# Kernel optimization log

Hardware: AMD Instinct MI355X
Metric: run time of the kernel (lower is better)

## Reference

```python
import jax, jax.numpy as jnp
import numpy as np

H = 32          # num query heads
KV = 8          # num kv heads
D = 64          # head_dim
WIN = 512       # sliding_window
BASE = 10000.0  # rope base


def setup_inputs() -> dict:
    key = jax.random.key(0)
    ks = jax.random.split(key, 5)
    B, S, DIM = 2, 2048, 2048
    x = jax.random.normal(ks[0], (B, S, DIM), dtype=jnp.float32)
    wq = jax.random.normal(ks[1], (H * D, DIM), dtype=jnp.float32) * 0.02
    wk = jax.random.normal(ks[2], (KV * D, DIM), dtype=jnp.float32) * 0.02
    wv = jax.random.normal(ks[3], (KV * D, DIM), dtype=jnp.float32) * 0.02
    wo = jax.random.normal(ks[4], (DIM, H * D), dtype=jnp.float32) * 0.02
    return {"x": x, "wq": wq, "wk": wk, "wv": wv, "wo": wo}


def _rope_tables(S):
    inv_freq = 1.0 / (BASE ** (jnp.arange(0, D, 2, dtype=jnp.float32) / D))
    t = jnp.arange(S, dtype=jnp.float32)
    freqs = t[:, None] * inv_freq[None, :]          # [S, D/2]
    emb = jnp.concatenate([freqs, freqs], axis=-1)  # [S, D]
    return jnp.cos(emb)[:, None, :], jnp.sin(emb)[:, None, :]  # [S,1,D]


def _rotate_half(u):
    return jnp.concatenate([-u[..., D // 2:], u[..., :D // 2]], axis=-1)


def reference(x, wq, wk, wv, wo):
    B, S, _ = x.shape
    q = (x @ wq.T).reshape(B, S, H, D)
    k = (x @ wk.T).reshape(B, S, KV, D)
    v = (x @ wv.T).reshape(B, S, KV, D)

    cos, sin = _rope_tables(S)  # [S,1,D] broadcasts over batch and heads
    q = q * cos + _rotate_half(q) * sin
    k = k * cos + _rotate_half(k) * sin

    q = q.transpose(0, 2, 1, 3)                        # [B,H,S,D]
    k = jnp.repeat(k.transpose(0, 2, 1, 3), H // KV, axis=1)  # [B,H,S,D]
    v = jnp.repeat(v.transpose(0, 2, 1, 3), H // KV, axis=1)

    scale = 1.0 / jnp.sqrt(jnp.float32(D))
    scores = jnp.einsum('bhqd,bhkd->bhqk', q, k) * scale  # [B,H,S,S]

    i = jnp.arange(S)[:, None]
    j = jnp.arange(S)[None, :]
    window_mask = jnp.abs(i - j) > WIN // 2   # True = masked (outside window)
    causal_mask = j > i                        # True = masked (future)
    masked = window_mask | causal_mask
    scores = jnp.where(masked[None, None], -jnp.inf, scores)

    attn = jax.nn.softmax(scores, axis=-1)
    out = jnp.einsum('bhqk,bhkd->bhqd', attn, v)  # [B,H,S,D]
    out = out.transpose(0, 2, 1, 3).reshape(B, S, H * D)
    return out @ wo.T
```

## Files before the change

kernel.cpp:

```cpp
#include <hip/hip_runtime.h>
#include <cstdint>
#include <cstddef>

#define SLEN 2048
#define NB 2
#define NH 32
#define NKV 8
#define HD 64
#define MROWS 4096
#define QDIM 2048
#define KVDIM 512
#define WINH 256

typedef float f32x4 __attribute__((ext_vector_type(4)));
typedef __bf16 bf16x8 __attribute__((ext_vector_type(8)));

__device__ __forceinline__ unsigned short f2bf(float f) {
  union { float f; unsigned u; } v; v.f = f;
  unsigned r = v.u + 0x7fffu + ((v.u >> 16) & 1u);
  return (unsigned short)(r >> 16);
}
__device__ __forceinline__ float bf2f(unsigned short h) {
  union { unsigned u; float f; } v; v.u = ((unsigned)h) << 16;
  return v.f;
}
__device__ __forceinline__ unsigned pk2(float a, float b) {
  return (unsigned)f2bf(a) | ((unsigned)f2bf(b) << 16);
}
__device__ __forceinline__ uint4 cvt16(float4 a, float4 b) {
  uint4 u;
  u.x = pk2(a.x, a.y); u.y = pk2(a.z, a.w);
  u.z = pk2(b.x, b.y); u.w = pk2(b.z, b.w);
  return u;
}
__device__ __forceinline__ void async16(const unsigned short* g, unsigned short* l) {
  __builtin_amdgcn_global_load_lds(
      (const __attribute__((address_space(1))) unsigned int*)g,
      (__attribute__((address_space(3))) unsigned int*)l, 16, 0, 0);
}

__global__ void rope_table(float2* __restrict__ tab) {
  int tid = blockIdx.x * 256 + threadIdx.x;
  int d = tid & 31;
  int s = tid >> 5;
  float inv = expf((float)d * (-2.0f / 64.0f) * 9.210340371976184f);
  float ang = (float)s * inv;
  float sn, cs;
  sincosf(ang, &sn, &cs);
  tab[tid] = make_float2(cs, sn);
}

__global__ void conv_bf16(const float* __restrict__ src, unsigned short* __restrict__ dst) {
  size_t t = (size_t)blockIdx.x * 256 + threadIdx.x;
  float4 a = *(const float4*)(src + t * 8);
  float4 b = *(const float4*)(src + t * 8 + 4);
  *(uint4*)(dst + t * 8) = cvt16(a, b);
}

__global__ void conv_wqkv(const float* __restrict__ wq, const float* __restrict__ wk,
                          const float* __restrict__ wv, unsigned short* __restrict__ dst) {
  size_t t = (size_t)blockIdx.x * 256 + threadIdx.x;
  size_t e = t * 8;
  int row = (int)(e >> 11);
  const float* src; size_t off;
  if (row < 2048)       { src = wq; off = e; }
  else if (row < 2560)  { src = wk; off = e - (size_t)2048 * 2048; }
  else                  { src = wv; off = e - (size_t)2560 * 2048; }
  float4 a = *(const float4*)(src + off);
  float4 b = *(const float4*)(src + off + 4);
  *(uint4*)(dst + e) = cvt16(a, b);
}

__global__ __launch_bounds__(512, 2) void qkv_gemm(
    const unsigned short* __restrict__ Ap, const unsigned short* __restrict__ Bp,
    const float* __restrict__ tabf,
    unsigned short* __restrict__ o_q, unsigned short* __restrict__ o_k,
    unsigned short* __restrict__ o_v)
{
  extern __shared__ unsigned short L[];
  constexpr int NT = 32;

  const int bid = blockIdx.x;
  const int swz = (bid & 7) * 24 + (bid >> 3);
  const int bm0 = (swz & 15) * 256;
  const int bn0 = (swz >> 4) * 256;

  const int tid = threadIdx.x;
  const int lane = tid & 63, wid = tid >> 6;
  const int g = lane >> 4, cl = lane & 15;
  const int wm = wid >> 2, wn = wid & 3;

  const int r0 = wid * 32 + (lane >> 2);
  const int s0 = (((lane & 3) ^ ((lane >> 3) & 3)) << 3);
  const unsigned short* gA = Ap + (size_t)(bm0 + r0) * 2048 + s0;
  const unsigned short* gB = Bp + (size_t)(bn0 + r0) * 2048 + s0;

  const int slotus = ((g ^ ((cl >> 1) & 3)) << 3);
  const int aread = (wm * 128 + cl) * 32 + slotus;
  const int bread = (wn * 64 + cl) * 32 + slotus;

#define REG_(b, op, kh) ((((b) * 2 + (op)) * 2 + (kh)) * 8192)
#define STG(op, kh, tt, db) do { \
    const unsigned short* s_ = ((op) ? gB : gA) + (tt) * 64 + (kh) * 32; \
    unsigned short* d_ = L + REG_(db, op, kh) + wid * 1024; \
    async16(s_, d_); \
    async16(s_ + 16 * 2048, d_ + 512); \
  } while (0)
#define LDA(dst, kh, mh) \
    _Pragma("unroll") for (int mf = 0; mf < 4; ++mf) \
      dst[mf] = *(const bf16x8*)&L[REG_(cb, 0, kh) + aread + (mh) * 2048 + mf * 512];
#define LDB(dst, kh) \
    _Pragma("unroll") for (int nf = 0; nf < 4; ++nf) \
      dst[nf] = *(const bf16x8*)&L[REG_(cb, 1, kh) + bread + nf * 512];
#define MM(mh, A, B) do { \
    __builtin_amdgcn_s_setprio(1); \
    _Pragma("unroll") for (int mf = 0; mf < 4; ++mf) \
      _Pragma("unroll") for (int nf = 0; nf < 4; ++nf) \
        acc[(mh) * 4 + mf][nf] = __builtin_amdgcn_mfma_f32_16x16x32_bf16( \
            A[mf], B[nf], acc[(mh) * 4 + mf][nf], 0, 0, 0); \
    __builtin_amdgcn_s_setprio(0); \
  } while (0)

  f32x4 acc[8][4] = {};

  STG(0, 0, 0, 0); STG(1, 0, 0, 0); STG(0, 1, 0, 0); STG(1, 1, 0, 0);
  STG(0, 0, 1, 1); STG(1, 0, 1, 1);
  asm volatile("s_waitcnt vmcnt(4)" ::: "memory");
  __builtin_amdgcn_s_barrier();
  __builtin_amdgcn_sched_barrier(0);

#pragma unroll 1
  for (int t = 0; t < NT; ++t) {
    const int cb = t & 1, nb = cb ^ 1;
    bf16x8 a00[4], a10[4], a01[4], a11[4], b0[4], b1[4];

    if (t + 1 < NT) STG(0, 1, t + 1, nb);
    LDA(a00, 0, 0); LDB(b0, 0);
    if (t + 1 < NT) STG(1, 1, t + 1, nb);
    LDA(a10, 0, 1);
    MM(0, a00, b0);
    LDA(a01, 1, 0); LDB(b1, 1);
    MM(1, a10, b0);
    asm volatile("s_waitcnt lgkmcnt(0)" ::: "memory");
    __builtin_amdgcn_s_barrier();
    __builtin_amdgcn_sched_barrier(0);
    if (t + 2 < NT) STG(0, 0, t + 2, cb);
    LDA(a11, 1, 1);
    MM(0, a01, b1);
    if (t + 2 < NT) STG(1, 0, t + 2, cb);
    MM(1, a11, b1);
    if (t + 2 < NT) { asm volatile("s_waitcnt vmcnt(4)" ::: "memory"); }
    else            { asm volatile("s_waitcnt vmcnt(0)" ::: "memory"); }
    asm volatile("s_waitcnt lgkmcnt(0)" ::: "memory");
    __builtin_amdgcn_s_barrier();
    __builtin_amdgcn_sched_barrier(0);
  }
#undef MM
#undef LDB
#undef LDA
#undef STG
#undef REG_

  const int rb = bm0 + wm * 128;
  const float2* tab = (const float2*)tabf;
  if (bn0 < QDIM) {
    const int colb = bn0 + wn * 64;
#pragma unroll
    for (int m = 0; m < 8; ++m)
#pragma unroll
      for (int nf = 0; nf < 2; ++nf) {
        const int d = nf * 16 + cl;
#pragma unroll
        for (int p = 0; p < 4; ++p) {
          int row = rb + m * 16 + g * 4 + p;
          int s = row & (SLEN - 1);
          float2 cs = tab[s * 32 + d];
          float a = acc[m][nf][p], b2 = acc[m][nf + 2][p];
          o_q[(size_t)row * QDIM + colb + d]      = f2bf(a * cs.x - b2 * cs.y);
          o_q[(size_t)row * QDIM + colb + d + 32] = f2bf(b2 * cs.x + a * cs.y);
        }
      }
  } else if (bn0 < QDIM + KVDIM) {
    const int colb = bn0 - QDIM + wn * 64;
#pragma unroll
    for (int m = 0; m < 8; ++m)
#pragma unroll
      for (int nf = 0; nf < 2; ++nf) {
        const int d = nf * 16 + cl;
#pragma unroll
        for (int p = 0; p < 4; ++p) {
          int row = rb + m * 16 + g * 4 + p;
          int s = row & (SLEN - 1);
          float2 cs = tab[s * 32 + d];
          float a = acc[m][nf][p], b2 = acc[m][nf + 2][p];
          o_k[(size_t)row * KVDIM + colb + d]      = f2bf(a * cs.x - b2 * cs.y);
          o_k[(size_t)row * KVDIM + colb + d + 32] = f2bf(b2 * cs.x + a * cs.y);
        }
      }
  } else {
    const int colb = bn0 - QDIM - KVDIM + wn * 64;
#pragma unroll
    for (int m = 0; m < 8; ++m)
#pragma unroll
      for (int nf = 0; nf < 4; ++nf) {
        int col = colb + nf * 16 + cl;
        int kvh = col >> 6, d = col & 63;
        int row0 = rb + m * 16 + g * 4;
        int bb = row0 >> 11, s = row0 & (SLEN - 1);
        unsigned short* dst = o_v + (((size_t)(bb * NKV + kvh) * HD + d) << 11) + s;
        uint2 u;
        u.x = pk2(acc[m][nf][0], acc[m][nf][1]);
        u.y = pk2(acc[m][nf][2], acc[m][nf][3]);
        *(uint2*)dst = u;
      }
  }
}

__global__ __launch_bounds__(512, 2) void out_gemm(
    const unsigned short* __restrict__ Ap, const unsigned short* __restrict__ Bp,
    float* __restrict__ o_f)
{
  extern __shared__ unsigned short L[];
  constexpr int NT = 32;

  const int bid = blockIdx.x;
  const int swz = (bid & 7) * 32 + (bid >> 3);
  const int bm0 = (swz & 31) * 128;
  const int bn0 = (swz >> 5) * 256;

  const int tid = threadIdx.x;
  const int lane = tid & 63, wid = tid >> 6;
  const int g = lane >> 4, cl = lane & 15;
  const int wm = wid >> 2, wn = wid & 3;

  const int s0 = (((lane & 3) ^ ((lane >> 3) & 3)) << 3);
  const unsigned short* gA = Ap + (size_t)(bm0 + wid * 16 + (lane >> 2)) * 2048 + s0;
  const unsigned short* gB = Bp + (size_t)(bn0 + wid * 32 + (lane >> 2)) * 2048 + s0;

  const int slotus = ((g ^ ((cl >> 1) & 3)) << 3);
  const int aread = (wm * 64 + cl) * 32 + slotus;
  const int bread = (wn * 64 + cl) * 32 + slotus;

#define REGA_(b, kh) ((b) * 24576 + (kh) * 4096)
#define REGB_(b, kh) ((b) * 24576 + 8192 + (kh) * 8192)
#define STGA(kh, tt, db) \
    async16(gA + (tt) * 64 + (kh) * 32, L + REGA_(db, kh) + wid * 512)
#define STGB(kh, tt, db) do { \
    const unsigned short* s_ = gB + (tt) * 64 + (kh) * 32; \
    unsigned short* d_ = L + REGB_(db, kh) + wid * 1024; \
    async16(s_, d_); \
    async16(s_ + 16 * 2048, d_ + 512); \
  } while (0)
#define LA(dst, kh, mp) \
    _Pragma("unroll") for (int mf = 0; mf < 2; ++mf) \
      dst[mf] = *(const bf16x8*)&L[REGA_(cb, kh) + aread + (mp) * 1024 + mf * 512];
#define LB(dst, kh) \
    _Pragma("unroll") for (int nf = 0; nf < 4; ++nf) \
      dst[nf] = *(const bf16x8*)&L[REGB_(cb, kh) + bread + nf * 512];
#define MMO(mp, A, B) do { \
    __builtin_amdgcn_s_setprio(1); \
    _Pragma("unroll") for (int mf = 0; mf < 2; ++mf) \
      _Pragma("unroll") for (int nf = 0; nf < 4; ++nf) \
        acc[(mp) * 2 + mf][nf] = __builtin_amdgcn_mfma_f32_16x16x32_bf16( \
            A[mf], B[nf], acc[(mp) * 2 + mf][nf], 0, 0, 0); \
    __builtin_amdgcn_s_setprio(0); \
  } while (0)

  f32x4 acc[4][4] = {};

  STGA(0, 0, 0); STGB(0, 0, 0); STGA(1, 0, 0); STGB(1, 0, 0);
  STGA(0, 1, 1); STGB(0, 1, 1);
  asm volatile("s_waitcnt vmcnt(3)" ::: "memory");
  __builtin_amdgcn_s_barrier();
  __builtin_amdgcn_sched_barrier(0);

#pragma unroll 1
  for (int t = 0; t < NT; ++t) {
    const int cb = t & 1, nb = cb ^ 1;
    bf16x8 p00[2], p10[2], p01[2], p11[2], b0[4], b1[4];

    if (t + 1 < NT) STGA(1, t + 1, nb);
    LA(p00, 0, 0); LB(b0, 0);
    if (t + 1 < NT) STGB(1, t + 1, nb);
    LA(p10, 0, 1);
    MMO(0, p00, b0);
    LA(p01, 1, 0); LB(b1, 1);
    MMO(1, p10, b0);
    asm volatile("s_waitcnt lgkmcnt(0)" ::: "memory");
    __builtin_amdgcn_s_barrier();
    __builtin_amdgcn_sched_barrier(0);
    if (t + 2 < NT) STGA(0, t + 2, cb);
    LA(p11, 1, 1);
    MMO(0, p01, b1);
    if (t + 2 < NT) STGB(0, t + 2, cb);
    MMO(1, p11, b1);
    if (t + 2 < NT) { asm volatile("s_waitcnt vmcnt(3)" ::: "memory"); }
    else            { asm volatile("s_waitcnt vmcnt(0)" ::: "memory"); }
    asm volatile("s_waitcnt lgkmcnt(0)" ::: "memory");
    __builtin_amdgcn_s_barrier();
    __builtin_amdgcn_sched_barrier(0);
  }
#undef MMO
#undef LB
#undef LA
#undef STGB
#undef STGA
#undef REGB_
#undef REGA_

  const int rb = bm0 + wm * 64;
  const int colb = bn0 + wn * 64;
#pragma unroll
  for (int m = 0; m < 4; ++m)
#pragma unroll
    for (int nf = 0; nf < 4; ++nf)
#pragma unroll
      for (int p = 0; p < 4; ++p) {
        int row = rb + m * 16 + g * 4 + p;
        o_f[(size_t)row * 2048 + colb + nf * 16 + cl] = acc[m][nf][p];
      }
}

__global__ __launch_bounds__(256) void attn(
    const unsigned short* __restrict__ qb, const unsigned short* __restrict__ kb,
    const unsigned short* __restrict__ vt, unsigned short* __restrict__ ao)
{
  __shared__ __align__(16) unsigned short Plds[4][16][40];
  const int lane = threadIdx.x & 63, wid = threadIdx.x >> 6;
  const int g = lane >> 4, cl = lane & 15;
  const int qt = blockIdx.x * 4 + wid;
  const int bh = qt >> 7, tl = qt & 127;
  const int i0 = tl * 16;
  const int b = bh >> 5, h = bh & 31, kvh = (bh & 31) >> 2;
  const int qi = i0 + cl;

  const unsigned short* qp = qb + ((size_t)(b * SLEN + i0 + cl) * NH + h) * HD + g * 8;
  bf16x8 qf0 = *(const bf16x8*)qp;
  bf16x8 qf1 = *(const bf16x8*)(qp + 32);

  f32x4 acc_o[4] = {};
  float m_run = -1e30f, l_run = 0.f;
  int jb = i0 - WINH; if (jb < 0) jb = 0;

  for (int j0 = jb; j0 <= i0; j0 += 32) {
    f32x4 sacc[2];
#pragma unroll
    for (int t = 0; t < 2; ++t) {
      int krow = j0 + 16 * t + cl;
      if (krow > SLEN - 1) krow = SLEN - 1;
      const unsigned short* kp = kb + ((size_t)(b * SLEN + krow) * NKV + kvh) * HD + g * 8;
      bf16x8 kf0 = *(const bf16x8*)kp;
      bf16x8 kf1 = *(const bf16x8*)(kp + 32);
      f32x4 z = {};
      z = __builtin_amdgcn_mfma_f32_16x16x32_bf16(kf0, qf0, z, 0, 0, 0);
      z = __builtin_amdgcn_mfma_f32_16x16x32_bf16(kf1, qf1, z, 0, 0, 0);
      sacc[t] = z;
    }
    float s[2][4];
    float mx = -1e30f;
#pragma unroll
    for (int t = 0; t < 2; ++t)
#pragma unroll
      for (int p = 0; p < 4; ++p) {
        int kj = j0 + 16 * t + g * 4 + p;
        bool ok = (kj <= qi) && (qi - kj <= WINH);
        float v = ok ? sacc[t][p] * 0.125f : -1e30f;
        s[t][p] = v;
        mx = fmaxf(mx, v);
      }
    mx = fmaxf(mx, __shfl_xor(mx, 16));
    mx = fmaxf(mx, __shfl_xor(mx, 32));
    float mnew = fmaxf(m_run, mx);
    float corr = __expf(m_run - mnew);
    float ps = 0.f;
    unsigned pw[2][2];
#pragma unroll
    for (int t = 0; t < 2; ++t) {
      float p0 = __expf(s[t][0] - mnew);
      float p1 = __expf(s[t][1] - mnew);
      float p2 = __expf(s[t][2] - mnew);
      float p3 = __expf(s[t][3] - mnew);
      ps += p0 + p1 + p2 + p3;
      pw[t][0] = pk2(p0, p1);
      pw[t][1] = pk2(p2, p3);
    }
    ps += __shfl_xor(ps, 16);
    ps += __shfl_xor(ps, 32);
    l_run = l_run * corr + ps;
    m_run = mnew;
#pragma unroll
    for (int vbk = 0; vbk < 4; ++vbk)
#pragma unroll
      for (int p = 0; p < 4; ++p) acc_o[vbk][p] *= corr;
#pragma unroll
    for (int t = 0; t < 2; ++t) {
      *(unsigned*)&Plds[wid][cl][16 * t + 4 * g]     = pw[t][0];
      *(unsigned*)&Plds[wid][cl][16 * t + 4 * g + 2] = pw[t][1];
    }
    bf16x8 pf = *(const bf16x8*)&Plds[wid][cl][g * 8];
    int jv = j0 + g * 8;
    if (jv > SLEN - 8) jv = SLEN - 8;
    const unsigned short* vbase = vt + ((size_t)(b * NKV + kvh) * HD) * SLEN + jv;
#pragma unroll
    for (int vbk = 0; vbk < 4; ++vbk) {
      bf16x8 vf = *(const bf16x8*)(vbase + (size_t)(vbk * 16 + cl) * SLEN);
      acc_o[vbk] = __builtin_amdgcn_mfma_f32_16x16x32_bf16(vf, pf, acc_o[vbk], 0, 0, 0);
    }
  }
  float inv = 1.0f / l_run;
  unsigned short* op = ao + ((size_t)(b * SLEN + i0 + cl) * NH + h) * HD;
#pragma unroll
  for (int vbk = 0; vbk < 4; ++vbk) {
    unsigned u0 = pk2(acc_o[vbk][0] * inv, acc_o[vbk][1] * inv);
    unsigned u1 = pk2(acc_o[vbk][2] * inv, acc_o[vbk][3] * inv);
    *(unsigned*)(op + vbk * 16 + g * 4)     = u0;
    *(unsigned*)(op + vbk * 16 + g * 4 + 2) = u1;
  }
}

extern "C" void kernel_launch(void* const* d_in, const int* in_sizes, int n_in,
                              void* d_out, int out_size, void* d_ws, size_t ws_size,
                              hipStream_t stream) {
  const float* x  = (const float*)d_in[0];
  const float* wq = (const float*)d_in[1];
  const float* wk = (const float*)d_in[2];
  const float* wv = (const float*)d_in[3];
  const float* wo = (const float*)d_in[4];
  float* out = (float*)d_out;

  char* w = (char*)d_ws;
  unsigned short* wqkvb = (unsigned short*)w; w += (size_t)3072 * 2048 * 2;
  unsigned short* xb    = (unsigned short*)w; w += (size_t)MROWS * QDIM * 2;
  unsigned short* qb    = (unsigned short*)w; w += (size_t)MROWS * QDIM * 2;
  unsigned short* kb    = (unsigned short*)w; w += (size_t)MROWS * KVDIM * 2;
  unsigned short* vt    = (unsigned short*)w; w += (size_t)MROWS * KVDIM * 2;
  float* tab            = (float*)w;          w += (size_t)SLEN * 32 * 8;
  unsigned short* wob = wqkvb;
  unsigned short* ao  = xb;

  hipFuncSetAttribute((const void*)qkv_gemm,
                      hipFuncAttributeMaxDynamicSharedMemorySize, 131072);
  hipFuncSetAttribute((const void*)out_gemm,
                      hipFuncAttributeMaxDynamicSharedMemorySize, 98304);

  rope_table<<<SLEN * 32 / 256, 256, 0, stream>>>((float2*)tab);
  conv_bf16<<<(MROWS * 2048) / (8 * 256), 256, 0, stream>>>(x, xb);
  conv_wqkv<<<(3072 * 2048) / (8 * 256), 256, 0, stream>>>(wq, wk, wv, wqkvb);
  qkv_gemm<<<192, 512, 131072, stream>>>(xb, wqkvb, tab, qb, kb, vt);
  conv_bf16<<<(2048 * 2048) / (8 * 256), 256, 0, stream>>>(wo, wob);
  attn<<<(NB * NH * (SLEN / 16)) / 4, 256, 0, stream>>>(qb, kb, vt, ao);
  out_gemm<<<256, 512, 98304, stream>>>(ao, wob, out);
}
```

Baseline: 194.7 us.

## Shrink QKV and output GEMM tiles to 128x128 with 256-thread blocks

Both GEMMs move from 256x256 (QKV) and 128x256 (output) tiles with 512-thread blocks to uniform 128x128 tiles with 256-thread blocks and 64 KB LDS. This raises the grid from 192 and 256 blocks to 768 and 512, so the work fills all CUs of the MI355X more evenly. The inner loop is simplified to two A/B fragment loads per k-step, and one lgkmcnt wait is removed. The cost is less data reuse per tile, so each output element needs more global and LDS traffic.

```diff
diff --git a/kernel.cpp b/kernel.cpp
--- a/kernel.cpp
+++ b/kernel.cpp
@@ -71,7 +71,7 @@
   *(uint4*)(dst + e) = cvt16(a, b);
 }
 
-__global__ __launch_bounds__(512, 2) void qkv_gemm(
+__global__ __launch_bounds__(256, 2) void qkv_gemm(
     const unsigned short* __restrict__ Ap, const unsigned short* __restrict__ Bp,
     const float* __restrict__ tabf,
     unsigned short* __restrict__ o_q, unsigned short* __restrict__ o_k,
@@ -81,14 +81,14 @@
   constexpr int NT = 32;
 
   const int bid = blockIdx.x;
-  const int swz = (bid & 7) * 24 + (bid >> 3);
-  const int bm0 = (swz & 15) * 256;
-  const int bn0 = (swz >> 4) * 256;
+  const int swz = (bid & 7) * 96 + (bid >> 3);
+  const int bm0 = (swz & 31) * 128;
+  const int bn0 = (swz >> 5) * 128;
 
   const int tid = threadIdx.x;
   const int lane = tid & 63, wid = tid >> 6;
   const int g = lane >> 4, cl = lane & 15;
-  const int wm = wid >> 2, wn = wid & 3;
+  const int wm = wid >> 1, wn = wid & 1;
 
   const int r0 = wid * 32 + (lane >> 2);
   const int s0 = (((lane & 3) ^ ((lane >> 3) & 3)) << 3);
@@ -96,32 +96,32 @@
   const unsigned short* gB = Bp + (size_t)(bn0 + r0) * 2048 + s0;
 
   const int slotus = ((g ^ ((cl >> 1) & 3)) << 3);
-  const int aread = (wm * 128 + cl) * 32 + slotus;
+  const int aread = (wm * 64 + cl) * 32 + slotus;
   const int bread = (wn * 64 + cl) * 32 + slotus;
 
-#define REG_(b, op, kh) ((((b) * 2 + (op)) * 2 + (kh)) * 8192)
+#define REG_(b, op, kh) ((((b) * 2 + (op)) * 2 + (kh)) * 4096)
 #define STG(op, kh, tt, db) do { \
     const unsigned short* s_ = ((op) ? gB : gA) + (tt) * 64 + (kh) * 32; \
     unsigned short* d_ = L + REG_(db, op, kh) + wid * 1024; \
     async16(s_, d_); \
     async16(s_ + 16 * 2048, d_ + 512); \
   } while (0)
-#define LDA(dst, kh, mh) \
+#define LDA(dst, kh) \
     _Pragma("unroll") for (int mf = 0; mf < 4; ++mf) \
-      dst[mf] = *(const bf16x8*)&L[REG_(cb, 0, kh) + aread + (mh) * 2048 + mf * 512];
+      dst[mf] = *(const bf16x8*)&L[REG_(cb, 0, kh) + aread + mf * 512];
 #define LDB(dst, kh) \
     _Pragma("unroll") for (int nf = 0; nf < 4; ++nf) \
       dst[nf] = *(const bf16x8*)&L[REG_(cb, 1, kh) + bread + nf * 512];
-#define MM(mh, A, B) do { \
+#define MM(A, B) do { \
     __builtin_amdgcn_s_setprio(1); \
     _Pragma("unroll") for (int mf = 0; mf < 4; ++mf) \
       _Pragma("unroll") for (int nf = 0; nf < 4; ++nf) \
-        acc[(mh) * 4 + mf][nf] = __builtin_amdgcn_mfma_f32_16x16x32_bf16( \
-            A[mf], B[nf], acc[(mh) * 4 + mf][nf], 0, 0, 0); \
+        acc[mf][nf] = __builtin_amdgcn_mfma_f32_16x16x32_bf16( \
+            A[mf], B[nf], acc[mf][nf], 0, 0, 0); \
     __builtin_amdgcn_s_setprio(0); \
   } while (0)
 
-  f32x4 acc[8][4] = {};
+  f32x4 acc[4][4] = {};
 
   STG(0, 0, 0, 0); STG(1, 0, 0, 0); STG(0, 1, 0, 0); STG(1, 1, 0, 0);
   STG(0, 0, 1, 1); STG(1, 0, 1, 1);
@@ -132,26 +132,21 @@
 #pragma unroll 1
   for (int t = 0; t < NT; ++t) {
     const int cb = t & 1, nb = cb ^ 1;
-    bf16x8 a00[4], a10[4], a01[4], a11[4], b0[4], b1[4];
+    bf16x8 a0[4], a1[4], b0[4], b1[4];
 
     if (t + 1 < NT) STG(0, 1, t + 1, nb);
-    LDA(a00, 0, 0); LDB(b0, 0);
+    LDA(a0, 0); LDB(b0, 0);
     if (t + 1 < NT) STG(1, 1, t + 1, nb);
-    LDA(a10, 0, 1);
-    MM(0, a00, b0);
-    LDA(a01, 1, 0); LDB(b1, 1);
-    MM(1, a10, b0);
+    LDA(a1, 1); LDB(b1, 1);
+    MM(a0, b0);
     asm volatile("s_waitcnt lgkmcnt(0)" ::: "memory");
     __builtin_amdgcn_s_barrier();
     __builtin_amdgcn_sched_barrier(0);
     if (t + 2 < NT) STG(0, 0, t + 2, cb);
-    LDA(a11, 1, 1);
-    MM(0, a01, b1);
+    MM(a1, b1);
     if (t + 2 < NT) STG(1, 0, t + 2, cb);
-    MM(1, a11, b1);
     if (t + 2 < NT) { asm volatile("s_waitcnt vmcnt(4)" ::: "memory"); }
     else            { asm volatile("s_waitcnt vmcnt(0)" ::: "memory"); }
-    asm volatile("s_waitcnt lgkmcnt(0)" ::: "memory");
     __builtin_amdgcn_s_barrier();
     __builtin_amdgcn_sched_barrier(0);
   }
@@ -161,12 +156,12 @@
 #undef STG
 #undef REG_
 
-  const int rb = bm0 + wm * 128;
+  const int rb = bm0 + wm * 64;
   const float2* tab = (const float2*)tabf;
   if (bn0 < QDIM) {
     const int colb = bn0 + wn * 64;
 #pragma unroll
-    for (int m = 0; m < 8; ++m)
+    for (int m = 0; m < 4; ++m)
 #pragma unroll
       for (int nf = 0; nf < 2; ++nf) {
         const int d = nf * 16 + cl;
@@ -183,7 +178,7 @@
   } else if (bn0 < QDIM + KVDIM) {
     const int colb = bn0 - QDIM + wn * 64;
 #pragma unroll
-    for (int m = 0; m < 8; ++m)
+    for (int m = 0; m < 4; ++m)
 #pragma unroll
       for (int nf = 0; nf < 2; ++nf) {
         const int d = nf * 16 + cl;
@@ -200,7 +195,7 @@
   } else {
     const int colb = bn0 - QDIM - KVDIM + wn * 64;
 #pragma unroll
-    for (int m = 0; m < 8; ++m)
+    for (int m = 0; m < 4; ++m)
 #pragma unroll
       for (int nf = 0; nf < 4; ++nf) {
         int col = colb + nf * 16 + cl;
@@ -216,7 +211,7 @@
   }
 }
 
-__global__ __launch_bounds__(512, 2) void out_gemm(
+__global__ __launch_bounds__(256, 2) void out_gemm(
     const unsigned short* __restrict__ Ap, const unsigned short* __restrict__ Bp,
     float* __restrict__ o_f)
 {
@@ -224,89 +219,80 @@
   constexpr int NT = 32;
 
   const int bid = blockIdx.x;
-  const int swz = (bid & 7) * 32 + (bid >> 3);
+  const int swz = (bid & 7) * 64 + (bid >> 3);
   const int bm0 = (swz & 31) * 128;
-  const int bn0 = (swz >> 5) * 256;
+  const int bn0 = (swz >> 5) * 128;
 
   const int tid = threadIdx.x;
   const int lane = tid & 63, wid = tid >> 6;
   const int g = lane >> 4, cl = lane & 15;
-  const int wm = wid >> 2, wn = wid & 3;
-
+  const int wm = wid >> 1, wn = wid & 1;
+
+  const int r0 = wid * 32 + (lane >> 2);
   const int s0 = (((lane & 3) ^ ((lane >> 3) & 3)) << 3);
-  const unsigned short* gA = Ap + (size_t)(bm0 + wid * 16 + (lane >> 2)) * 2048 + s0;
-  const unsigned short* gB = Bp + (size_t)(bn0 + wid * 32 + (lane >> 2)) * 2048 + s0;
+  const unsigned short* gA = Ap + (size_t)(bm0 + r0) * 2048 + s0;
+  const unsigned short* gB = Bp + (size_t)(bn0 + r0) * 2048 + s0;
 
   const int slotus = ((g ^ ((cl >> 1) & 3)) << 3);
   const int aread = (wm * 64 + cl) * 32 + slotus;
   const int bread = (wn * 64 + cl) * 32 + slotus;
 
-#define REGA_(b, kh) ((b) * 24576 + (kh) * 4096)
-#define REGB_(b, kh) ((b) * 24576 + 8192 + (kh) * 8192)
-#define STGA(kh, tt, db) \
-    async16(gA + (tt) * 64 + (kh) * 32, L + REGA_(db, kh) + wid * 512)
-#define STGB(kh, tt, db) do { \
-    const unsigned short* s_ = gB + (tt) * 64 + (kh) * 32; \
-    unsigned short* d_ = L + REGB_(db, kh) + wid * 1024; \
+#define REG_(b, op, kh) ((((b) * 2 + (op)) * 2 + (kh)) * 4096)
+#define STG(op, kh, tt, db) do { \
+    const unsigned short* s_ = ((op) ? gB : gA) + (tt) * 64 + (kh) * 32; \
+    unsigned short* d_ = L + REG_(db, op, kh) + wid * 1024; \
     async16(s_, d_); \
     async16(s_ + 16 * 2048, d_ + 512); \
   } while (0)
-#define LA(dst, kh, mp) \
-    _Pragma("unroll") for (int mf = 0; mf < 2; ++mf) \
-      dst[mf] = *(const bf16x8*)&L[REGA_(cb, kh) + aread + (mp) * 1024 + mf * 512];
-#define LB(dst, kh) \
+#define LDA(dst, kh) \
+    _Pragma("unroll") for (int mf = 0; mf < 4; ++mf) \
+      dst[mf] = *(const bf16x8*)&L[REG_(cb, 0, kh) + aread + mf * 512];
+#define LDB(dst, kh) \
     _Pragma("unroll") for (int nf = 0; nf < 4; ++nf) \
-      dst[nf] = *(const bf16x8*)&L[REGB_(cb, kh) + bread + nf * 512];
-#define MMO(mp, A, B) do { \
+      dst[nf] = *(const bf16x8*)&L[REG_(cb, 1, kh) + bread + nf * 512];
+#define MM(A, B) do { \
     __builtin_amdgcn_s_setprio(1); \
-    _Pragma("unroll") for (int mf = 0; mf < 2; ++mf) \
+    _Pragma("unroll") for (int mf = 0; mf < 4; ++mf) \
       _Pragma("unroll") for (int nf = 0; nf < 4; ++nf) \
-        acc[(mp) * 2 + mf][nf] = __builtin_amdgcn_mfma_f32_16x16x32_bf16( \
-            A[mf], B[nf], acc[(mp) * 2 + mf][nf], 0, 0, 0); \
+        acc[mf][nf] = __builtin_amdgcn_mfma_f32_16x16x32_bf16( \
+            A[mf], B[nf], acc[mf][nf], 0, 0, 0); \
     __builtin_amdgcn_s_setprio(0); \
   } while (0)
 
   f32x4 acc[4][4] = {};
 
-  STGA(0, 0, 0); STGB(0, 0, 0); STGA(1, 0, 0); STGB(1, 0, 0);
-  STGA(0, 1, 1); STGB(0, 1, 1);
-  asm volatile("s_waitcnt vmcnt(3)" ::: "memory");
+  STG(0, 0, 0, 0); STG(1, 0, 0, 0); STG(0, 1, 0, 0); STG(1, 1, 0, 0);
+  STG(0, 0, 1, 1); STG(1, 0, 1, 1);
+  asm volatile("s_waitcnt vmcnt(4)" ::: "memory");
   __builtin_amdgcn_s_barrier();
   __builtin_amdgcn_sched_barrier(0);
 
 #pragma unroll 1
   for (int t = 0; t < NT; ++t) {
     const int cb = t & 1, nb = cb ^ 1;
-    bf16x8 p00[2], p10[2], p01[2], p11[2], b0[4], b1[4];
-
-    if (t + 1 < NT) STGA(1, t + 1, nb);
-    LA(p00, 0, 0); LB(b0, 0);
-    if (t + 1 < NT) STGB(1, t + 1, nb);
-    LA(p10, 0, 1);
-    MMO(0, p00, b0);
-    LA(p01, 1, 0); LB(b1, 1);
-    MMO(1, p10, b0);
+    bf16x8 a0[4], a1[4], b0[4], b1[4];
+
+    if (t + 1 < NT) STG(0, 1, t + 1, nb);
+    LDA(a0, 0); LDB(b0, 0);
+    if (t + 1 < NT) STG(1, 1, t + 1, nb);
+    LDA(a1, 1); LDB(b1, 1);
+    MM(a0, b0);
     asm volatile("s_waitcnt lgkmcnt(0)" ::: "memory");
     __builtin_amdgcn_s_barrier();
     __builtin_amdgcn_sched_barrier(0);
-    if (t + 2 < NT) STGA(0, t + 2, cb);
-    LA(p11, 1, 1);
-    MMO(0, p01, b1);
-    if (t + 2 < NT) STGB(0, t + 2, cb);
-    MMO(1, p11, b1);
-    if (t + 2 < NT) { asm volatile("s_waitcnt vmcnt(3)" ::: "memory"); }
+    if (t + 2 < NT) STG(0, 0, t + 2, cb);
+    MM(a1, b1);
+    if (t + 2 < NT) STG(1, 0, t + 2, cb);
+    if (t + 2 < NT) { asm volatile("s_waitcnt vmcnt(4)" ::: "memory"); }
     else            { asm volatile("s_waitcnt vmcnt(0)" ::: "memory"); }
-    asm volatile("s_waitcnt lgkmcnt(0)" ::: "memory");
     __builtin_amdgcn_s_barrier();
     __builtin_amdgcn_sched_barrier(0);
   }
-#undef MMO
-#undef LB
-#undef LA
-#undef STGB
-#undef STGA
-#undef REGB_
-#undef REGA_
+#undef MM
+#undef LDB
+#undef LDA
+#undef STG
+#undef REG_
 
   const int rb = bm0 + wm * 64;
   const int colb = bn0 + wn * 64;
@@ -439,15 +425,15 @@
   unsigned short* ao  = xb;
 
   hipFuncSetAttribute((const void*)qkv_gemm,
-                      hipFuncAttributeMaxDynamicSharedMemorySize, 131072);
+                      hipFuncAttributeMaxDynamicSharedMemorySize, 65536);
   hipFuncSetAttribute((const void*)out_gemm,
-                      hipFuncAttributeMaxDynamicSharedMemorySize, 98304);
+                      hipFuncAttributeMaxDynamicSharedMemorySize, 65536);
 
   rope_table<<<SLEN * 32 / 256, 256, 0, stream>>>((float2*)tab);
   conv_bf16<<<(MROWS * 2048) / (8 * 256), 256, 0, stream>>>(x, xb);
   conv_wqkv<<<(3072 * 2048) / (8 * 256), 256, 0, stream>>>(wq, wk, wv, wqkvb);
-  qkv_gemm<<<192, 512, 131072, stream>>>(xb, wqkvb, tab, qb, kb, vt);
+  qkv_gemm<<<768, 256, 65536, stream>>>(xb, wqkvb, tab, qb, kb, vt);
   conv_bf16<<<(2048 * 2048) / (8 * 256), 256, 0, stream>>>(wo, wob);
   attn<<<(NB * NH * (SLEN / 16)) / 4, 256, 0, stream>>>(qb, kb, vt, ao);
-  out_gemm<<<256, 512, 98304, stream>>>(ao, wob, out);
-}
+  out_gemm<<<512, 256, 65536, stream>>>(ao, wob, out);
+}
```

Result: slower. 206.9 us (+6.3%).

## Retile QKV GEMM to 192-wide N tiles and move RoPE to separate kernel

Applied to the files above, without the earlier changes.

The QKV projection GEMM now uses 192-column N tiles, so the grid grows from 192 to 256 blocks, one per compute unit on the device. This is meant to remove the idle compute units left by the old grid. Because a 48-column warp slice no longer holds both halves of a 64-wide head, the fused RoPE epilogue is replaced by plain bf16 stores plus a separate elementwise rope_qk kernel that rewrites Q and K in place. The cost is an extra kernel launch and an extra global read and write of Q and K. The B staging still loads 256 rows per tile, so the weight workspace is padded and about a quarter of the B traffic goes unused.

```diff
diff --git a/kernel.cpp b/kernel.cpp
--- a/kernel.cpp
+++ b/kernel.cpp
@@ -71,9 +71,37 @@
   *(uint4*)(dst + e) = cvt16(a, b);
 }
 
+__global__ void rope_qk(unsigned short* __restrict__ qb,
+                        unsigned short* __restrict__ kb,
+                        const float* __restrict__ tabf) {
+  const float2* tab = (const float2*)tabf;
+  int tid = blockIdx.x * 256 + threadIdx.x;
+  int oct = tid & 3;
+  int head = (tid >> 2) % 40;
+  int row = tid / 160;
+  int s = row & (SLEN - 1);
+  int d0 = oct * 8;
+  unsigned short* p = (head < NH)
+      ? qb + (size_t)row * QDIM + head * HD
+      : kb + (size_t)row * KVDIM + (head - NH) * HD;
+  uint4 u0 = *(const uint4*)(p + d0);
+  uint4 u1 = *(const uint4*)(p + d0 + 32);
+  const unsigned short* a16 = (const unsigned short*)&u0;
+  const unsigned short* b16 = (const unsigned short*)&u1;
+  unsigned short o0[8], o1[8];
+#pragma unroll
+  for (int j = 0; j < 8; ++j) {
+    float2 cs = tab[s * 32 + d0 + j];
+    float a = bf2f(a16[j]), b = bf2f(b16[j]);
+    o0[j] = f2bf(a * cs.x - b * cs.y);
+    o1[j] = f2bf(b * cs.x + a * cs.y);
+  }
+  *(uint4*)(p + d0)      = *(const uint4*)o0;
+  *(uint4*)(p + d0 + 32) = *(const uint4*)o1;
+}
+
 __global__ __launch_bounds__(512, 2) void qkv_gemm(
     const unsigned short* __restrict__ Ap, const unsigned short* __restrict__ Bp,
-    const float* __restrict__ tabf,
     unsigned short* __restrict__ o_q, unsigned short* __restrict__ o_k,
     unsigned short* __restrict__ o_v)
 {
@@ -81,9 +109,9 @@
   constexpr int NT = 32;
 
   const int bid = blockIdx.x;
-  const int swz = (bid & 7) * 24 + (bid >> 3);
+  const int swz = (bid & 7) * 32 + (bid >> 3);
   const int bm0 = (swz & 15) * 256;
-  const int bn0 = (swz >> 4) * 256;
+  const int bn0 = (swz >> 4) * 192;
 
   const int tid = threadIdx.x;
   const int lane = tid & 63, wid = tid >> 6;
@@ -97,7 +125,7 @@
 
   const int slotus = ((g ^ ((cl >> 1) & 3)) << 3);
   const int aread = (wm * 128 + cl) * 32 + slotus;
-  const int bread = (wn * 64 + cl) * 32 + slotus;
+  const int bread = (wn * 48 + cl) * 32 + slotus;
 
 #define REG_(b, op, kh) ((((b) * 2 + (op)) * 2 + (kh)) * 8192)
 #define STG(op, kh, tt, db) do { \
@@ -110,18 +138,18 @@
     _Pragma("unroll") for (int mf = 0; mf < 4; ++mf) \
       dst[mf] = *(const bf16x8*)&L[REG_(cb, 0, kh) + aread + (mh) * 2048 + mf * 512];
 #define LDB(dst, kh) \
-    _Pragma("unroll") for (int nf = 0; nf < 4; ++nf) \
+    _Pragma("unroll") for (int nf = 0; nf < 3; ++nf) \
       dst[nf] = *(const bf16x8*)&L[REG_(cb, 1, kh) + bread + nf * 512];
 #define MM(mh, A, B) do { \
     __builtin_amdgcn_s_setprio(1); \
     _Pragma("unroll") for (int mf = 0; mf < 4; ++mf) \
-      _Pragma("unroll") for (int nf = 0; nf < 4; ++nf) \
+      _Pragma("unroll") for (int nf = 0; nf < 3; ++nf) \
         acc[(mh) * 4 + mf][nf] = __builtin_amdgcn_mfma_f32_16x16x32_bf16( \
             A[mf], B[nf], acc[(mh) * 4 + mf][nf], 0, 0, 0); \
     __builtin_amdgcn_s_setprio(0); \
   } while (0)
 
-  f32x4 acc[8][4] = {};
+  f32x4 acc[8][3] = {};
 
   STG(0, 0, 0, 0); STG(1, 0, 0, 0); STG(0, 1, 0, 0); STG(1, 1, 0, 0);
   STG(0, 0, 1, 1); STG(1, 0, 1, 1);
@@ -132,7 +160,7 @@
 #pragma unroll 1
   for (int t = 0; t < NT; ++t) {
     const int cb = t & 1, nb = cb ^ 1;
-    bf16x8 a00[4], a10[4], a01[4], a11[4], b0[4], b1[4];
+    bf16x8 a00[4], a10[4], a01[4], a11[4], b0[3], b1[3];
 
     if (t + 1 < NT) STG(0, 1, t + 1, nb);
     LDA(a00, 0, 0); LDB(b0, 0);
@@ -162,49 +190,26 @@
 #undef REG_
 
   const int rb = bm0 + wm * 128;
-  const float2* tab = (const float2*)tabf;
-  if (bn0 < QDIM) {
-    const int colb = bn0 + wn * 64;
-#pragma unroll
-    for (int m = 0; m < 8; ++m)
-#pragma unroll
-      for (int nf = 0; nf < 2; ++nf) {
-        const int d = nf * 16 + cl;
+#pragma unroll
+  for (int m = 0; m < 8; ++m)
+#pragma unroll
+    for (int nf = 0; nf < 3; ++nf) {
+      const int col = bn0 + wn * 48 + nf * 16 + cl;
+      if (col < QDIM) {
 #pragma unroll
         for (int p = 0; p < 4; ++p) {
           int row = rb + m * 16 + g * 4 + p;
-          int s = row & (SLEN - 1);
-          float2 cs = tab[s * 32 + d];
-          float a = acc[m][nf][p], b2 = acc[m][nf + 2][p];
-          o_q[(size_t)row * QDIM + colb + d]      = f2bf(a * cs.x - b2 * cs.y);
-          o_q[(size_t)row * QDIM + colb + d + 32] = f2bf(b2 * cs.x + a * cs.y);
+          o_q[(size_t)row * QDIM + col] = f2bf(acc[m][nf][p]);
         }
-      }
-  } else if (bn0 < QDIM + KVDIM) {
-    const int colb = bn0 - QDIM + wn * 64;
-#pragma unroll
-    for (int m = 0; m < 8; ++m)
-#pragma unroll
-      for (int nf = 0; nf < 2; ++nf) {
-        const int d = nf * 16 + cl;
+      } else if (col < QDIM + KVDIM) {
 #pragma unroll
         for (int p = 0; p < 4; ++p) {
           int row = rb + m * 16 + g * 4 + p;
-          int s = row & (SLEN - 1);
-          float2 cs = tab[s * 32 + d];
-          float a = acc[m][nf][p], b2 = acc[m][nf + 2][p];
-          o_k[(size_t)row * KVDIM + colb + d]      = f2bf(a * cs.x - b2 * cs.y);
-          o_k[(size_t)row * KVDIM + colb + d + 32] = f2bf(b2 * cs.x + a * cs.y);
+          o_k[(size_t)row * KVDIM + col - QDIM] = f2bf(acc[m][nf][p]);
         }
-      }
-  } else {
-    const int colb = bn0 - QDIM - KVDIM + wn * 64;
-#pragma unroll
-    for (int m = 0; m < 8; ++m)
-#pragma unroll
-      for (int nf = 0; nf < 4; ++nf) {
-        int col = colb + nf * 16 + cl;
-        int kvh = col >> 6, d = col & 63;
+      } else {
+        int vc = col - QDIM - KVDIM;
+        int kvh = vc >> 6, d = vc & 63;
         int row0 = rb + m * 16 + g * 4;
         int bb = row0 >> 11, s = row0 & (SLEN - 1);
         unsigned short* dst = o_v + (((size_t)(bb * NKV + kvh) * HD + d) << 11) + s;
@@ -213,7 +218,7 @@
         u.y = pk2(acc[m][nf][2], acc[m][nf][3]);
         *(uint2*)dst = u;
       }
-  }
+    }
 }
 
 __global__ __launch_bounds__(512, 2) void out_gemm(
@@ -429,7 +434,7 @@
   float* out = (float*)d_out;
 
   char* w = (char*)d_ws;
-  unsigned short* wqkvb = (unsigned short*)w; w += (size_t)3072 * 2048 * 2;
+  unsigned short* wqkvb = (unsigned short*)w; w += (size_t)3136 * 2048 * 2;
   unsigned short* xb    = (unsigned short*)w; w += (size_t)MROWS * QDIM * 2;
   unsigned short* qb    = (unsigned short*)w; w += (size_t)MROWS * QDIM * 2;
   unsigned short* kb    = (unsigned short*)w; w += (size_t)MROWS * KVDIM * 2;
@@ -446,7 +451,8 @@
   rope_table<<<SLEN * 32 / 256, 256, 0, stream>>>((float2*)tab);
   conv_bf16<<<(MROWS * 2048) / (8 * 256), 256, 0, stream>>>(x, xb);
   conv_wqkv<<<(3072 * 2048) / (8 * 256), 256, 0, stream>>>(wq, wk, wv, wqkvb);
-  qkv_gemm<<<192, 512, 131072, stream>>>(xb, wqkvb, tab, qb, kb, vt);
+  qkv_gemm<<<256, 512, 131072, stream>>>(xb, wqkvb, qb, kb, vt);
+  rope_qk<<<(MROWS * 40 * 4) / 256, 256, 0, stream>>>(qb, kb, tab);
   conv_bf16<<<(2048 * 2048) / (8 * 256), 256, 0, stream>>>(wo, wob);
   attn<<<(NB * NH * (SLEN / 16)) / 4, 256, 0, stream>>>(qb, kb, vt, ao);
   out_gemm<<<256, 512, 98304, stream>>>(ao, wob, out);
```

Measured after the change: 196.9 us. About the same (+1.2%).
